# Performance work log

Measured on AMD Instinct MI355X. Metric: run time of the kernel, lower is better.

## Reference

```python
import jax, jax.numpy as jnp
import numpy as np

BITS = 4
GROUP_SIZE = 128
MAXQ = (1 << BITS) - 1  # 15
PACK = 32 // BITS       # 8 nibbles per int32


def setup_inputs() -> dict:
    key = jax.random.key(0)
    k1, k2, k3, k4, k5 = jax.random.split(key, 5)
    infeatures, outfeatures, tokens = 8192, 8192, 4096
    n_groups = infeatures // GROUP_SIZE  # 64
    x = jax.random.normal(k1, (tokens, infeatures), dtype=jnp.float32)
    qweight = jax.random.randint(k2, (infeatures // PACK, outfeatures), 0, 2147483647, dtype=jnp.int32)
    qzeros = jax.random.randint(k3, (n_groups, outfeatures // PACK), 0, 2147483647, dtype=jnp.int32)
    scales = jax.random.uniform(k4, (n_groups, outfeatures), dtype=jnp.float32) * 0.01 + 0.001
    bias = jax.random.normal(k5, (outfeatures,), dtype=jnp.float32)
    return {"x": x, "qweight": qweight, "qzeros": qzeros, "scales": scales, "bias": bias}


def _dequant(qweight, qzeros, scales):
    shifts = jnp.arange(0, 32, BITS, dtype=jnp.int32)  # [8]
    # unpack weight nibbles: [in/8, 8, out] -> [n_groups, group_size, out]
    w = (qweight[:, None, :] >> shifts[None, :, None]) & MAXQ
    w = w.reshape(-1, GROUP_SIZE, qweight.shape[1])
    # unpack zero points: [ng, out/8, 8] -> [ng, out]; note stored as (zero-1)
    z = ((qzeros[:, :, None] >> shifts[None, None, :]) & MAXQ) + 1
    z = z.reshape(z.shape[0], -1)
    # groupwise dequant: scales * (w - z)
    W = scales[:, None, :] * (w.astype(scales.dtype) - z[:, None, :].astype(scales.dtype))
    return W.reshape(-1, W.shape[-1])  # [infeatures, outfeatures]


def reference(x, qweight, qzeros, scales, bias):
    W = _dequant(qweight, qzeros, scales)
    return x @ W + bias
```

## Files before the change

### kernel.cpp

```cpp
#include <hip/hip_runtime.h>
#include <hip/hip_bf16.h>

constexpr int MM = 4096;
constexpr int NN = 8192;
constexpr int KK = 8192;
constexpr int BM = 256, BN = 256, BK = 64;
constexpr int THREADS = 512;
constexpr int NKB = KK / BK;
constexpr int NT = NN / BN;

typedef __bf16 bf16;
typedef __attribute__((ext_vector_type(8))) __bf16 bf16x8;
typedef __attribute__((ext_vector_type(4))) float floatx4;

__device__ __forceinline__ void async_copy16(const void* g, void* l) {
    __builtin_amdgcn_global_load_lds(
        (const __attribute__((address_space(1))) void*)g,
        (__attribute__((address_space(3))) void*)l, 16, 0, 0);
}

__global__ __launch_bounds__(256)
void convert_x(const float* __restrict__ x, bf16* __restrict__ xb) {
    const int tid = blockIdx.x * 256 + threadIdx.x;
    const int c = tid & 7;
    const int m = (tid >> 3) & 255;
    const int kb = (tid >> 11) & 127;
    const int mtile = tid >> 18;
    const int row = mtile * 256 + m;
    const int col = kb * 64 + c * 8;
    const float4* src = (const float4*)(x + (size_t)row * KK + col);
    const float4 f0 = src[0];
    const float4 f1 = src[1];
    bf16x8 v;
    v[0] = (bf16)f0.x; v[1] = (bf16)f0.y; v[2] = (bf16)f0.z; v[3] = (bf16)f0.w;
    v[4] = (bf16)f1.x; v[5] = (bf16)f1.y; v[6] = (bf16)f1.z; v[7] = (bf16)f1.w;
    const int dst_chunk = (tid & ~7) | (c ^ (m & 7));
    *(bf16x8*)(xb + (size_t)dst_chunk * 8) = v;
}

__global__ __launch_bounds__(THREADS, 2)
void qgemm_dma(const bf16* __restrict__ xb,
               const unsigned* __restrict__ qweight,
               const unsigned* __restrict__ qzeros,
               const float* __restrict__ scales,
               const float* __restrict__ bias,
               float* __restrict__ out)
{
    __shared__ alignas(16) bf16 As[2][BM * BK];
    __shared__ alignas(16) bf16 Bs[2][BN * BK];

    const int t = threadIdx.x;
    const int ntile = blockIdx.x & (NT - 1);
    const int mtile = blockIdx.x / NT;
    const int n0 = ntile * BN;

    const int wave = t >> 6;
    const int lane = t & 63;
    const int wm = (wave >> 1) * 64;
    const int wn = (wave & 1) * 128;
    const int ml = lane & 15;
    const int quad = lane >> 4;

    const int bn = t & 255;
    const int rbase = (t >> 8) * 4;
    const int gn = n0 + bn;

    floatx4 acc[4][8];
#pragma unroll
    for (int i = 0; i < 4; ++i)
#pragma unroll
        for (int j = 0; j < 8; ++j)
            acc[i][j] = (floatx4){0.f, 0.f, 0.f, 0.f};

    const char* xb_base = (const char*)xb
        + (size_t)mtile * NKB * (BM * BK) * sizeof(bf16);

    unsigned bq[4];
    float s = 0.f, sz = 0.f;

    auto stage_a = [&](int kb, int buf) {
        const char* g = xb_base + (size_t)kb * (BM * BK * 2) + wave * 4096 + lane * 16;
        char* l = (char*)&As[buf][0] + wave * 4096;
#pragma unroll
        for (int i = 0; i < 4; ++i)
            async_copy16(g + i * 1024, l + i * 1024);
    };
    auto load_b = [&](int kb) {
#pragma unroll
        for (int i = 0; i < 4; ++i)
            bq[i] = qweight[(size_t)(kb * 8 + rbase + i) * NN + gn];
    };
    auto store_b = [&](int buf) {
#pragma unroll
        for (int i = 0; i < 4; ++i) {
            const int rq = rbase + i;
            bf16x8 v;
#pragma unroll
            for (int j = 0; j < 8; ++j)
                v[j] = (bf16)((float)((bq[i] >> (4 * j)) & 15u) * s - sz);
            *(bf16x8*)&Bs[buf][bn * BK + ((rq ^ (bn & 7)) << 3)] = v;
        }
    };
    auto compute = [&](int buf) {
#pragma unroll
        for (int ks = 0; ks < 2; ++ks) {
            const int clog = ks * 4 + quad;
            bf16x8 af[4];
#pragma unroll
            for (int im = 0; im < 4; ++im) {
                const int row = wm + im * 16 + ml;
                af[im] = *(const bf16x8*)&As[buf][row * BK + ((clog ^ (row & 7)) << 3)];
            }
#pragma unroll
            for (int jh = 0; jh < 2; ++jh) {
                bf16x8 bf4[4];
#pragma unroll
                for (int j = 0; j < 4; ++j) {
                    const int row = wn + (jh * 4 + j) * 16 + ml;
                    bf4[j] = *(const bf16x8*)&Bs[buf][row * BK + ((clog ^ (row & 7)) << 3)];
                }
#pragma unroll
                for (int im = 0; im < 4; ++im)
#pragma unroll
                    for (int j = 0; j < 4; ++j)
                        acc[im][jh * 4 + j] = __builtin_amdgcn_mfma_f32_16x16x32_bf16(
                            af[im], bf4[j], acc[im][jh * 4 + j], 0, 0, 0);
            }
        }
    };

    {
        s = scales[gn];
        const unsigned zw = qzeros[gn >> 3];
        sz = s * (float)(((zw >> (4 * (gn & 7))) & 15u) + 1u);
        stage_a(0, 0);
        load_b(0);
        store_b(0);
    }
    __syncthreads();

    float s_nxt = 0.f;
    unsigned zw_nxt = 0;
    for (int kb = 0; kb < NKB; ++kb) {
        const int p = kb & 1, q = p ^ 1;
        const bool has_next = (kb + 1) < NKB;
        if (has_next) {
            stage_a(kb + 1, q);
            load_b(kb + 1);
            if (((kb + 1) & 1) == 0) {
                const int g = (kb + 1) >> 1;
                s_nxt = scales[(size_t)g * NN + gn];
                zw_nxt = qzeros[(size_t)g * (NN / 8) + (gn >> 3)];
            }
        }
        compute(p);
        if (has_next) {
            if (((kb + 1) & 1) == 0) {
                s = s_nxt;
                sz = s * (float)(((zw_nxt >> (4 * (gn & 7))) & 15u) + 1u);
            }
            store_b(q);
            __syncthreads();
        }
    }

#pragma unroll
    for (int jn = 0; jn < 8; ++jn) {
        const int ngl = n0 + wn + jn * 16 + ml;
        const float bv = bias[ngl];
#pragma unroll
        for (int im = 0; im < 4; ++im) {
            const int mg = mtile * BM + wm + im * 16 + quad * 4;
#pragma unroll
            for (int r = 0; r < 4; ++r)
                out[(size_t)(mg + r) * NN + ngl] = acc[im][jn][r] + bv;
        }
    }
}

__global__ __launch_bounds__(THREADS, 2)
void qgemm_fallback(const float* __restrict__ x,
                    const unsigned* __restrict__ qweight,
                    const unsigned* __restrict__ qzeros,
                    const float* __restrict__ scales,
                    const float* __restrict__ bias,
                    float* __restrict__ out)
{
    __shared__ bf16 As[BM * BK];
    __shared__ bf16 Bs[BN * BK];

    const int t = threadIdx.x;
    const int ntile = blockIdx.x & 31;
    const int mtile = blockIdx.x >> 5;
    const int m0 = mtile * BM;
    const int n0 = ntile * BN;
    const int wave = t >> 6;
    const int lane = t & 63;
    const int wm = (wave >> 1) * 64;
    const int wn = (wave & 1) * 128;
    const int ml = lane & 15;
    const int quad = lane >> 4;
    const int bn = t & 255;
    const int rbase = (t >> 8) * 4;
    const int gn = n0 + bn;

    floatx4 acc[4][8];
    for (int i = 0; i < 4; ++i)
        for (int j = 0; j < 8; ++j)
            acc[i][j] = (floatx4){0.f, 0.f, 0.f, 0.f};

    float s = 0.f, sz = 0.f;

    for (int kb = 0; kb < KK / BK; ++kb) {
        const int k0 = kb * BK;
        if ((kb & 1) == 0) {
            const int g = kb >> 1;
            s = scales[g * NN + gn];
            const unsigned zw = qzeros[g * (NN / 8) + (gn >> 3)];
            const float z = (float)(((zw >> (4 * (gn & 7))) & 15u) + 1u);
            sz = s * z;
        }
#pragma unroll
        for (int i = 0; i < 4; ++i) {
            const int chunk = t + THREADS * i;
            const int m = chunk >> 3;
            const int c = chunk & 7;
            const float4* src = (const float4*)(x + (size_t)(m0 + m) * KK + (k0 + c * 8));
            const float4 f0 = src[0];
            const float4 f1 = src[1];
            bf16x8 v;
            v[0] = (bf16)f0.x; v[1] = (bf16)f0.y; v[2] = (bf16)f0.z; v[3] = (bf16)f0.w;
            v[4] = (bf16)f1.x; v[5] = (bf16)f1.y; v[6] = (bf16)f1.z; v[7] = (bf16)f1.w;
            *(bf16x8*)&As[m * BK + ((c ^ (m & 7)) << 3)] = v;
        }
        const int kq0 = k0 >> 3;
#pragma unroll
        for (int i = 0; i < 4; ++i) {
            const int rq = rbase + i;
            const unsigned q = qweight[(size_t)(kq0 + rq) * NN + gn];
            bf16x8 v;
#pragma unroll
            for (int j = 0; j < 8; ++j) {
                const float f = (float)((q >> (4 * j)) & 15u) * s - sz;
                v[j] = (bf16)f;
            }
            *(bf16x8*)&Bs[bn * BK + ((rq ^ (bn & 7)) << 3)] = v;
        }
        __syncthreads();
#pragma unroll
        for (int ks = 0; ks < 2; ++ks) {
            const int clog = ks * 4 + quad;
            bf16x8 af[4];
            bf16x8 bfr[8];
#pragma unroll
            for (int im = 0; im < 4; ++im) {
                const int row = wm + im * 16 + ml;
                af[im] = *(const bf16x8*)&As[row * BK + ((clog ^ (row & 7)) << 3)];
            }
#pragma unroll
            for (int jn = 0; jn < 8; ++jn) {
                const int row = wn + jn * 16 + ml;
                bfr[jn] = *(const bf16x8*)&Bs[row * BK + ((clog ^ (row & 7)) << 3)];
            }
#pragma unroll
            for (int im = 0; im < 4; ++im)
#pragma unroll
                for (int jn = 0; jn < 8; ++jn)
                    acc[im][jn] = __builtin_amdgcn_mfma_f32_16x16x32_bf16(
                        af[im], bfr[jn], acc[im][jn], 0, 0, 0);
        }
        __syncthreads();
    }
#pragma unroll
    for (int jn = 0; jn < 8; ++jn) {
        const int ngl = n0 + wn + jn * 16 + ml;
        const float bv = bias[ngl];
#pragma unroll
        for (int im = 0; im < 4; ++im) {
            const int mg = m0 + wm + im * 16 + quad * 4;
#pragma unroll
            for (int r = 0; r < 4; ++r)
                out[(size_t)(mg + r) * NN + ngl] = acc[im][jn][r] + bv;
        }
    }
}

extern "C" void kernel_launch(void* const* d_in, const int* in_sizes, int n_in,
                              void* d_out, int out_size, void* d_ws, size_t ws_size,
                              hipStream_t stream) {
    const float*    x       = (const float*)d_in[0];
    const unsigned* qweight = (const unsigned*)d_in[1];
    const unsigned* qzeros  = (const unsigned*)d_in[2];
    const float*    scales  = (const float*)d_in[3];
    const float*    bias    = (const float*)d_in[4];
    float* out = (float*)d_out;

    const int grid = (MM / BM) * (NN / BN);
    const size_t xb_bytes = (size_t)MM * KK * sizeof(bf16);

    if (ws_size >= xb_bytes) {
        bf16* xb = (bf16*)d_ws;
        const int chunks = MM * KK / 8;
        convert_x<<<chunks / 256, 256, 0, stream>>>(x, xb);
        qgemm_dma<<<grid, THREADS, 0, stream>>>(xb, qweight, qzeros, scales, bias, out);
    } else {
        qgemm_fallback<<<grid, THREADS, 0, stream>>>(x, qweight, qzeros, scales, bias, out);
    }
}
```

Measured before the change: 752.6 us.

## Dequantize weights in registers with fp16 magic-number trick, drop B LDS staging

The weight tile is no longer dequantized into shared memory. Each wave loads packed int4 words straight into registers and dequantizes them using the 0x6400 fp16 magic-number trick with packed half2 add and multiply, then feeds fp16 MFMAs directly. Activations are converted to fp16 with an interleaved nibble order, and the B-side LDS buffer and its store and read traffic are removed. The cost is redundant dequant work across waves that share columns, many more global loads per wave, fp16 range and precision risk for the activations, and s_setprio hints added for scheduling.

Result: slower. 1.726 ms (+129.3%).

```diff
diff --git a/kernel.cpp b/kernel.cpp
--- a/kernel.cpp
+++ b/kernel.cpp
@@ -9,9 +9,13 @@
 constexpr int NKB = KK / BK;
 constexpr int NT = NN / BN;
 
+typedef _Float16 f16;
+typedef __attribute__((ext_vector_type(2))) _Float16 f16x2;
+typedef __attribute__((ext_vector_type(8))) _Float16 f16x8;
+typedef __attribute__((ext_vector_type(4))) float floatx4;
+typedef __attribute__((ext_vector_type(4))) int intx4;
 typedef __bf16 bf16;
 typedef __attribute__((ext_vector_type(8))) __bf16 bf16x8;
-typedef __attribute__((ext_vector_type(4))) float floatx4;
 
 __device__ __forceinline__ void async_copy16(const void* g, void* l) {
     __builtin_amdgcn_global_load_lds(
@@ -20,7 +24,7 @@
 }
 
 __global__ __launch_bounds__(256)
-void convert_x(const float* __restrict__ x, bf16* __restrict__ xb) {
+void convert_x(const float* __restrict__ x, f16* __restrict__ xb) {
     const int tid = blockIdx.x * 256 + threadIdx.x;
     const int c = tid & 7;
     const int m = (tid >> 3) & 255;
@@ -31,23 +35,24 @@
     const float4* src = (const float4*)(x + (size_t)row * KK + col);
     const float4 f0 = src[0];
     const float4 f1 = src[1];
-    bf16x8 v;
-    v[0] = (bf16)f0.x; v[1] = (bf16)f0.y; v[2] = (bf16)f0.z; v[3] = (bf16)f0.w;
-    v[4] = (bf16)f1.x; v[5] = (bf16)f1.y; v[6] = (bf16)f1.z; v[7] = (bf16)f1.w;
+    f16x8 v;
+    v[0] = (f16)f0.x; v[1] = (f16)f1.x;
+    v[2] = (f16)f0.y; v[3] = (f16)f1.y;
+    v[4] = (f16)f0.z; v[5] = (f16)f1.z;
+    v[6] = (f16)f0.w; v[7] = (f16)f1.w;
     const int dst_chunk = (tid & ~7) | (c ^ (m & 7));
-    *(bf16x8*)(xb + (size_t)dst_chunk * 8) = v;
+    *(f16x8*)(xb + (size_t)dst_chunk * 8) = v;
 }
 
 __global__ __launch_bounds__(THREADS, 2)
-void qgemm_dma(const bf16* __restrict__ xb,
-               const unsigned* __restrict__ qweight,
-               const unsigned* __restrict__ qzeros,
-               const float* __restrict__ scales,
-               const float* __restrict__ bias,
-               float* __restrict__ out)
+void qgemm(const f16* __restrict__ xb,
+           const unsigned* __restrict__ qweight,
+           const unsigned* __restrict__ qzeros,
+           const float* __restrict__ scales,
+           const float* __restrict__ bias,
+           float* __restrict__ out)
 {
-    __shared__ alignas(16) bf16 As[2][BM * BK];
-    __shared__ alignas(16) bf16 Bs[2][BN * BK];
+    __shared__ alignas(16) f16 As[2][BM * BK];
 
     const int t = threadIdx.x;
     const int ntile = blockIdx.x & (NT - 1);
@@ -61,9 +66,9 @@
     const int ml = lane & 15;
     const int quad = lane >> 4;
 
-    const int bn = t & 255;
-    const int rbase = (t >> 8) * 4;
-    const int gn = n0 + bn;
+    const int colb = n0 + wn + ml;
+    const unsigned qcol = (unsigned)colb + (unsigned)quad * NN;
+    const int zsh = 4 * (ml & 7);
 
     floatx4 acc[4][8];
 #pragma unroll
@@ -72,11 +77,13 @@
         for (int j = 0; j < 8; ++j)
             acc[i][j] = (floatx4){0.f, 0.f, 0.f, 0.f};
 
+    unsigned bq[16];
+    unsigned s_pk[8], nzp[8];
+    float    s_raw[8];
+    unsigned zp_stage = 0;
+
     const char* xb_base = (const char*)xb
-        + (size_t)mtile * NKB * (BM * BK) * sizeof(bf16);
-
-    unsigned bq[4];
-    float s = 0.f, sz = 0.f;
+        + (size_t)mtile * NKB * (BM * BK) * sizeof(f16);
 
     auto stage_a = [&](int kb, int buf) {
         const char* g = xb_base + (size_t)kb * (BM * BK * 2) + wave * 4096 + lane * 16;
@@ -85,84 +92,104 @@
         for (int i = 0; i < 4; ++i)
             async_copy16(g + i * 1024, l + i * 1024);
     };
-    auto load_b = [&](int kb) {
-#pragma unroll
-        for (int i = 0; i < 4; ++i)
-            bq[i] = qweight[(size_t)(kb * 8 + rbase + i) * NN + gn];
-    };
-    auto store_b = [&](int buf) {
-#pragma unroll
-        for (int i = 0; i < 4; ++i) {
-            const int rq = rbase + i;
-            bf16x8 v;
-#pragma unroll
-            for (int j = 0; j < 8; ++j)
-                v[j] = (bf16)((float)((bq[i] >> (4 * j)) & 15u) * s - sz);
-            *(bf16x8*)&Bs[buf][bn * BK + ((rq ^ (bn & 7)) << 3)] = v;
-        }
-    };
-    auto compute = [&](int buf) {
-#pragma unroll
-        for (int ks = 0; ks < 2; ++ks) {
+
+    auto load_af = [&](int buf, int ks, f16x8 (&af)[4]) {
+#pragma unroll
+        for (int im = 0; im < 4; ++im) {
+            const int r = wm + im * 16 + ml;
             const int clog = ks * 4 + quad;
-            bf16x8 af[4];
-#pragma unroll
-            for (int im = 0; im < 4; ++im) {
-                const int row = wm + im * 16 + ml;
-                af[im] = *(const bf16x8*)&As[buf][row * BK + ((clog ^ (row & 7)) << 3)];
-            }
-#pragma unroll
-            for (int jh = 0; jh < 2; ++jh) {
-                bf16x8 bf4[4];
-#pragma unroll
-                for (int j = 0; j < 4; ++j) {
-                    const int row = wn + (jh * 4 + j) * 16 + ml;
-                    bf4[j] = *(const bf16x8*)&Bs[buf][row * BK + ((clog ^ (row & 7)) << 3)];
-                }
-#pragma unroll
-                for (int im = 0; im < 4; ++im)
-#pragma unroll
-                    for (int j = 0; j < 4; ++j)
-                        acc[im][jh * 4 + j] = __builtin_amdgcn_mfma_f32_16x16x32_bf16(
-                            af[im], bf4[j], acc[im][jh * 4 + j], 0, 0, 0);
-            }
-        }
-    };
-
-    {
-        s = scales[gn];
-        const unsigned zw = qzeros[gn >> 3];
-        sz = s * (float)(((zw >> (4 * (gn & 7))) & 15u) + 1u);
-        stage_a(0, 0);
-        load_b(0);
-        store_b(0);
-    }
+            af[im] = *(const f16x8*)&As[buf][r * BK + ((clog ^ (r & 7)) << 3)];
+        }
+    };
+
+    auto load_bq = [&](int kb, int ks, int jh) {
+        const unsigned rowoff = (unsigned)(kb * 8 + ks * 4) * NN;
+#pragma unroll
+        for (int j = 0; j < 4; ++j) {
+            const int jn = jh * 4 + j;
+            bq[ks * 8 + jn] = qweight[rowoff + qcol + jn * 16];
+        }
+    };
+
+    auto group_fetch = [&](int g) {
+#pragma unroll
+        for (int jn = 0; jn < 8; ++jn)
+            s_raw[jn] = scales[(unsigned)(g * NN) + (unsigned)(colb + jn * 16)];
+        unsigned zp = 0;
+#pragma unroll
+        for (int jn = 0; jn < 8; ++jn) {
+            const unsigned u = qzeros[(unsigned)(g * (NN / 8)) + (unsigned)((colb + jn * 16) >> 3)];
+            zp |= ((u >> zsh) & 15u) << (4 * jn);
+        }
+        zp_stage = zp;
+    };
+    auto group_convert = [&]() {
+#pragma unroll
+        for (int jn = 0; jn < 8; ++jn) {
+            const unsigned short sh = __builtin_bit_cast(unsigned short, (f16)s_raw[jn]);
+            s_pk[jn] = ((unsigned)sh << 16) | sh;
+            const unsigned nh = 0xE401u + ((zp_stage >> (4 * jn)) & 15u);
+            nzp[jn] = (nh << 16) | nh;
+        }
+    };
+
+    auto phase = [&](int ks, int jh, const f16x8 (&af)[4]) {
+        __builtin_amdgcn_s_setprio(1);
+#pragma unroll
+        for (int j = 0; j < 4; ++j) {
+            const int jn = jh * 4 + j;
+            const unsigned u = bq[ks * 8 + jn];
+            const unsigned t0 = ( u         & 0x000F000Fu) | 0x64006400u;
+            const unsigned t1 = ((u >> 4)   & 0x000F000Fu) | 0x64006400u;
+            const unsigned t2 = ((u >> 8)   & 0x000F000Fu) | 0x64006400u;
+            const unsigned t3 = ((u >> 12)  & 0x000F000Fu) | 0x64006400u;
+            const f16x2 z2 = __builtin_bit_cast(f16x2, nzp[jn]);
+            const f16x2 sp = __builtin_bit_cast(f16x2, s_pk[jn]);
+            const f16x2 w0 = (__builtin_bit_cast(f16x2, t0) + z2) * sp;
+            const f16x2 w1 = (__builtin_bit_cast(f16x2, t1) + z2) * sp;
+            const f16x2 w2 = (__builtin_bit_cast(f16x2, t2) + z2) * sp;
+            const f16x2 w3 = (__builtin_bit_cast(f16x2, t3) + z2) * sp;
+            const intx4 bi = { __builtin_bit_cast(int, w0), __builtin_bit_cast(int, w1),
+                               __builtin_bit_cast(int, w2), __builtin_bit_cast(int, w3) };
+            const f16x8 bfr = __builtin_bit_cast(f16x8, bi);
+#pragma unroll
+            for (int im = 0; im < 4; ++im)
+                acc[im][jn] = __builtin_amdgcn_mfma_f32_16x16x32_f16(
+                    af[im], bfr, acc[im][jn], 0, 0, 0);
+        }
+        __builtin_amdgcn_s_setprio(0);
+    };
+
+    auto body = [&](int kb, int buf, bool stage, bool odd) {
+        f16x8 af[4];
+        if (!odd && kb > 0) group_convert();
+        if (stage) stage_a(kb + 1, buf ^ 1);
+        load_af(buf, 0, af);
+        phase(0, 0, af);
+        if (stage) load_bq(kb + 1, 0, 0);
+        phase(0, 1, af);
+        if (stage) load_bq(kb + 1, 0, 1);
+        if (stage && odd) group_fetch((kb + 1) >> 1);
+        load_af(buf, 1, af);
+        phase(1, 0, af);
+        if (stage) load_bq(kb + 1, 1, 0);
+        phase(1, 1, af);
+        if (stage) load_bq(kb + 1, 1, 1);
+        if (stage) __syncthreads();
+    };
+
+    group_fetch(0);
+    group_convert();
+    stage_a(0, 0);
+    load_bq(0, 0, 0); load_bq(0, 0, 1); load_bq(0, 1, 0); load_bq(0, 1, 1);
     __syncthreads();
 
-    float s_nxt = 0.f;
-    unsigned zw_nxt = 0;
-    for (int kb = 0; kb < NKB; ++kb) {
-        const int p = kb & 1, q = p ^ 1;
-        const bool has_next = (kb + 1) < NKB;
-        if (has_next) {
-            stage_a(kb + 1, q);
-            load_b(kb + 1);
-            if (((kb + 1) & 1) == 0) {
-                const int g = (kb + 1) >> 1;
-                s_nxt = scales[(size_t)g * NN + gn];
-                zw_nxt = qzeros[(size_t)g * (NN / 8) + (gn >> 3)];
-            }
-        }
-        compute(p);
-        if (has_next) {
-            if (((kb + 1) & 1) == 0) {
-                s = s_nxt;
-                sz = s * (float)(((zw_nxt >> (4 * (gn & 7))) & 15u) + 1u);
-            }
-            store_b(q);
-            __syncthreads();
-        }
-    }
+    for (int kb = 0; kb < NKB - 2; kb += 2) {
+        body(kb, 0, true, false);
+        body(kb + 1, 1, true, true);
+    }
+    body(NKB - 2, 0, true, false);
+    body(NKB - 1, 1, false, true);
 
 #pragma unroll
     for (int jn = 0; jn < 8; ++jn) {
@@ -296,13 +323,13 @@
     float* out = (float*)d_out;
 
     const int grid = (MM / BM) * (NN / BN);
-    const size_t xb_bytes = (size_t)MM * KK * sizeof(bf16);
+    const size_t xb_bytes = (size_t)MM * KK * sizeof(f16);
 
     if (ws_size >= xb_bytes) {
-        bf16* xb = (bf16*)d_ws;
+        f16* xb = (f16*)d_ws;
         const int chunks = MM * KK / 8;
         convert_x<<<chunks / 256, 256, 0, stream>>>(x, xb);
-        qgemm_dma<<<grid, THREADS, 0, stream>>>(xb, qweight, qzeros, scales, bias, out);
+        qgemm<<<grid, THREADS, 0, stream>>>(xb, qweight, qzeros, scales, bias, out);
     } else {
         qgemm_fallback<<<grid, THREADS, 0, stream>>>(x, qweight, qzeros, scales, bias, out);
     }
```
